# Kernel optimization log

Measured on AMD Instinct MI355X. Metric: run time of the kernel, lower is better.

The kernel has to match this reference:

```python
import jax, jax.numpy as jnp
import numpy as np

D = 256      # embedding_dim
DI = 512     # inner dim = proj_factor * D
H = 4        # num heads
DH = DI // H # head dim
L = 4        # num blocks
K = 4        # causal conv kernel size

def _ln(x, g, b):
    mu = jnp.mean(x, -1, keepdims=True)
    v = jnp.var(x, -1, keepdims=True)
    return (x - mu) * jax.lax.rsqrt(v + 1e-5) * g + b

def _causal_conv(x, w, b):
    # x [B,S,DI], w [K,DI] depthwise causal conv
    S = x.shape[1]
    xp = jnp.pad(x, ((0, 0), (K - 1, 0), (0, 0)))
    out = b
    for j in range(K):
        out = out + xp[:, j:j + S, :] * w[j]
    return out

def _mlstm(q, k, v, ip, fp):
    # parallel stabilized mLSTM. q,k,v [B,S,H,DH]; ip,fp [B,S,H]
    q = q.transpose(0, 2, 1, 3)
    k = k.transpose(0, 2, 1, 3)
    v = v.transpose(0, 2, 1, 3)
    ip = ip.transpose(0, 2, 1)  # [B,H,S]
    fp = fp.transpose(0, 2, 1)
    lf = jax.nn.log_sigmoid(fp)                      # log forget gates
    Fc = jnp.cumsum(lf, axis=-1)
    Fc = jnp.concatenate([jnp.zeros_like(Fc[..., :1]), Fc], axis=-1)  # [B,H,S+1]
    logfg = Fc[..., 1:, None] - Fc[..., None, 1:]    # [B,H,S,S]: sum of log f over (s,t]
    S_len = q.shape[2]
    tri = jnp.tril(jnp.ones((S_len, S_len), dtype=bool))
    logD = jnp.where(tri, logfg + ip[..., None, :], jnp.float32(-1e30))
    m = jnp.max(logD, axis=-1, keepdims=True)        # stabilizer
    Dm = jnp.exp(logD - m)
    qk = jnp.einsum('bhtd,bhsd->bhts', q, k) * (DH ** -0.5)
    C = qk * Dm
    norm = jnp.maximum(jnp.abs(jnp.sum(C, axis=-1, keepdims=True)), jnp.exp(-m))
    h = jnp.einsum('bhts,bhsd->bhtd', C / (norm + 1e-6), v)
    return h.transpose(0, 2, 1, 3)

def _forward(x, time_features, Wp, bp, ln_g, ln_b, Wup, bup, conv_w, conv_b,
             Wq, Wk, Wv, Wif, bif, gn_g, gn_b, skip, Wdown, bdown,
             lnf_g, lnf_b, Wf, bf):
    B, S = x.shape
    xi = jnp.concatenate([x[..., None], time_features], axis=-1)  # [B,S,5]
    h = xi @ Wp + bp                                              # [B,S,D]
    for l in range(L):
        res = h
        hn = _ln(h, ln_g[l], ln_b[l])
        up = hn @ Wup[l] + bup[l]                 # [B,S,2*DI]
        xm, z = up[..., :DI], up[..., DI:]
        xc = jax.nn.silu(_causal_conv(xm, conv_w[l], conv_b[l]))
        q = (xc @ Wq[l]).reshape(B, S, H, DH)
        k = (xc @ Wk[l]).reshape(B, S, H, DH)
        v = (xm @ Wv[l]).reshape(B, S, H, DH)
        gi = jnp.concatenate([q.reshape(B, S, DI), k.reshape(B, S, DI), v.reshape(B, S, DI)], axis=-1)
        gates = gi @ Wif[l] + bif[l]              # [B,S,2H]
        ht = _mlstm(q, k, v, gates[..., :H], gates[..., H:])  # [B,S,H,DH]
        ht = _ln(ht, gn_g[l].reshape(H, DH), gn_b[l].reshape(H, DH)).reshape(B, S, DI)
        ht = ht + skip[l] * xc
        ht = ht * jax.nn.silu(z)
        h = res + ht @ Wdown[l] + bdown[l]
    h = _ln(h, lnf_g, lnf_b)
    return h[:, -1, :] @ Wf + bf                  # [B,1]

def setup_inputs():
    key = jax.random.key(0)
    ks = jax.random.split(key, 16)
    B, S = 8, 1024
    sd = jnp.float32(0.02)
    return {
        'x': jax.random.normal(ks[0], (B, S), jnp.float32),
        'time_features': jax.random.normal(ks[1], (B, S, 4), jnp.float32),
        'Wp': jax.random.normal(ks[2], (5, D)) * sd, 'bp': jnp.zeros((D,)),
        'ln_g': jnp.ones((L, D)), 'ln_b': jnp.zeros((L, D)),
        'Wup': jax.random.normal(ks[3], (L, D, 2 * DI)) * sd, 'bup': jnp.zeros((L, 2 * DI)),
        'conv_w': jax.random.normal(ks[4], (L, K, DI)) * sd, 'conv_b': jnp.zeros((L, DI)),
        'Wq': jax.random.normal(ks[5], (L, DI, DI)) * sd,
        'Wk': jax.random.normal(ks[6], (L, DI, DI)) * sd,
        'Wv': jax.random.normal(ks[7], (L, DI, DI)) * sd,
        'Wif': jax.random.normal(ks[8], (L, 3 * DI, 2 * H)) * sd, 'bif': jnp.zeros((L, 2 * H)),
        'gn_g': jnp.ones((L, DI)), 'gn_b': jnp.zeros((L, DI)),
        'skip': jnp.ones((L, DI)),
        'Wdown': jax.random.normal(ks[9], (L, DI, D)) * sd, 'bdown': jnp.zeros((L, D)),
        'lnf_g': jnp.ones((D,)), 'lnf_b': jnp.zeros((D,)),
        'Wf': jax.random.normal(ks[10], (D, 1)) * sd, 'bf': jnp.zeros((1,)),
    }

def reference(x, time_features, Wp, bp, ln_g, ln_b, Wup, bup, conv_w, conv_b,
              Wq, Wk, Wv, Wif, bif, gn_g, gn_b, skip, Wdown, bdown,
              lnf_g, lnf_b, Wf, bf):
    return _forward(x, time_features, Wp, bp, ln_g, ln_b, Wup, bup, conv_w, conv_b,
                    Wq, Wk, Wv, Wif, bif, gn_g, gn_b, skip, Wdown, bdown,
                    lnf_g, lnf_b, Wf, bf)
```

## Files before the change

### kernel.cpp

```cpp
#include <hip/hip_runtime.h>
#include <hip/hip_bf16.h>
#include <math.h>

#define S 1024
#define NLAYER 4

typedef __bf16 bf16x8 __attribute__((ext_vector_type(8)));
typedef float floatx4 __attribute__((ext_vector_type(4)));

__device__ __forceinline__ float wave_sum(float v) {
  #pragma unroll
  for (int off = 32; off > 0; off >>= 1) v += __shfl_xor(v, off, 64);
  return v;
}

__device__ __forceinline__ void wtrans_body(
    int bid, const float* Wup, const float* Wq, const float* Wk, const float* Wv,
    const float* Wdown, __bf16* WupT, __bf16* WqkT, __bf16* WvT, __bf16* WdownT) {
  __shared__ float T[32][33];
  int layer = bid / 1152, rr = bid % 1152;
  const float* src; __bf16* dst; int K, N, tile;
  if (rr < 256)       { src = Wup   + layer * 262144; dst = WupT  + layer * 262144;          K = 256; N = 1024; tile = rr; }
  else if (rr < 512)  { src = Wq    + layer * 262144; dst = WqkT  + layer * 524288;          K = 512; N = 512;  tile = rr - 256; }
  else if (rr < 768)  { src = Wk    + layer * 262144; dst = WqkT  + layer * 524288 + 262144; K = 512; N = 512;  tile = rr - 512; }
  else if (rr < 1024) { src = Wv    + layer * 262144; dst = WvT   + layer * 262144;          K = 512; N = 512;  tile = rr - 768; }
  else                { src = Wdown + layer * 131072; dst = WdownT + layer * 131072;         K = 512; N = 256;  tile = rr - 1024; }
  int ntn = N >> 5;
  int tk = tile / ntn, tn = tile % ntn;
  int tid = threadIdx.x;
  int r = tid >> 3, c4 = (tid & 7) * 4;
  float4 v = *(const float4*)(src + (size_t)(tk * 32 + r) * N + tn * 32 + c4);
  T[c4 + 0][r] = v.x; T[c4 + 1][r] = v.y; T[c4 + 2][r] = v.z; T[c4 + 3][r] = v.w;
  __syncthreads();
  __bf16 o[4];
  #pragma unroll
  for (int j = 0; j < 4; ++j) o[j] = (__bf16)T[r][c4 + j];
  *(uint2*)(dst + (size_t)(tn * 32 + r) * K + tk * 32 + c4) = *(uint2*)o;
}

__device__ __forceinline__ void wgprep_body(
    int bid, const float* Wq, const float* Wk, const float* Wv,
    const float* Wif, float* wg) {
  int l = bid >> 8;
  int rem = bid & 255;
  int sel = rem >> 7;
  int kg = rem & 127;
  int tid = threadIdx.x;
  int wv = tid >> 6, lane = tid & 63;
  int k = kg * 4 + wv;
  const float* wif = Wif + (size_t)l * 1536 * 8;
  float part[8] = {0, 0, 0, 0, 0, 0, 0, 0};
  if (sel == 0) {
    const float* qr = Wq + (size_t)l * 262144 + (size_t)k * 512;
    const float* kr = Wk + (size_t)l * 262144 + (size_t)k * 512;
    #pragma unroll
    for (int i = 0; i < 8; ++i) {
      int n = lane + i * 64;
      float qv = qr[n], kv = kr[n];
      const float* wq8 = wif + (size_t)n * 8;
      const float* wk8 = wif + (size_t)(512 + n) * 8;
      #pragma unroll
      for (int j = 0; j < 8; ++j) part[j] += qv * wq8[j] + kv * wk8[j];
    }
  } else {
    const float* vr = Wv + (size_t)l * 262144 + (size_t)k * 512;
    #pragma unroll
    for (int i = 0; i < 8; ++i) {
      int n = lane + i * 64;
      float vv = vr[n];
      const float* wv8 = wif + (size_t)(1024 + n) * 8;
      #pragma unroll
      for (int j = 0; j < 8; ++j) part[j] += vv * wv8[j];
    }
  }
  #pragma unroll
  for (int j = 0; j < 8; ++j) part[j] = wave_sum(part[j]);
  if (lane < 8) wg[(size_t)l * 8192 + sel * 4096 + (size_t)k * 8 + lane] = part[lane];
}

__device__ __forceinline__ void embed_body(
    int row, const float* x, const float* tf, const float* Wp, const float* bp,
    const float* g, const float* b, float* h, __bf16* hn) {
  int n = threadIdx.x;
  float xv = x[row];
  const float* t4 = tf + (size_t)row * 4;
  float acc = bp[n] + xv * Wp[n];
  acc += t4[0] * Wp[256 + n];
  acc += t4[1] * Wp[512 + n];
  acc += t4[2] * Wp[768 + n];
  acc += t4[3] * Wp[1024 + n];
  h[(size_t)row * 256 + n] = acc;
  __shared__ float red[4];
  int wid = n >> 6, lane = n & 63;
  float s = wave_sum(acc);
  if (lane == 0) red[wid] = s;
  __syncthreads();
  float mu = (red[0] + red[1] + red[2] + red[3]) * (1.f / 256.f);
  __syncthreads();
  float d = acc - mu;
  float s2 = wave_sum(d * d);
  if (lane == 0) red[wid] = s2;
  __syncthreads();
  float var = (red[0] + red[1] + red[2] + red[3]) * (1.f / 256.f);
  float rs = rsqrtf(var + 1e-5f);
  hn[(size_t)row * 256 + n] = (__bf16)(d * rs * g[n] + b[n]);
}

__global__ __launch_bounds__(256) void prep_kernel(
    const float* __restrict__ x, const float* __restrict__ tf,
    const float* __restrict__ Wp, const float* __restrict__ bp,
    const float* __restrict__ ln_g, const float* __restrict__ ln_b,
    const float* __restrict__ Wup, const float* __restrict__ Wq,
    const float* __restrict__ Wk, const float* __restrict__ Wv,
    const float* __restrict__ Wdown, const float* __restrict__ Wif,
    __bf16* __restrict__ WupT, __bf16* __restrict__ WqkT,
    __bf16* __restrict__ WvT, __bf16* __restrict__ WdownT,
    float* __restrict__ wg, float* __restrict__ h, __bf16* __restrict__ hn) {
  int bid = blockIdx.x;
  if (bid < 4608) {
    wtrans_body(bid, Wup, Wq, Wk, Wv, Wdown, WupT, WqkT, WvT, WdownT);
  } else if (bid < 4608 + 1024) {
    wgprep_body(bid - 4608, Wq, Wk, Wv, Wif, wg);
  } else {
    embed_body(bid - 5632, x, tf, Wp, bp, ln_g, ln_b, h, hn);
  }
}

template <int TM, int MODE, int ACC>
__device__ __forceinline__ void hgemm_body(
    char* smem_raw,
    const __bf16* __restrict__ A, int lda,
    const __bf16* __restrict__ BT, int Kdim,
    const float* __restrict__ bias,
    void* __restrict__ Cout, int ldc, int bxi, int byi) {
  auto As = (__bf16(*)[40])smem_raw;
  auto Bs = (__bf16(*)[40])(smem_raw + (size_t)TM * 80);
  int tid = threadIdx.x;
  int bm = bxi * TM, bn = byi * 128;
  int wid = tid >> 6, lane = tid & 63;
  int wr = wid >> 1, wc = wid & 1;
  int lg = lane >> 4, li = lane & 15;
  constexpr int MI = TM / 32;
  constexpr int WROW = TM / 2;
  floatx4 acc[MI][4];
  #pragma unroll
  for (int i = 0; i < MI; ++i)
    #pragma unroll
    for (int j = 0; j < 4; ++j) acc[i][j] = (floatx4)(0.f);

  int arow = tid >> 2, aseg = tid & 3;
  bf16x8 pa0, pa1, pb0, pb1;
  auto pre = [&](int k0) {
    pa0 = *(const bf16x8*)(A + (size_t)(bm + arow) * lda + k0 + aseg * 8);
    if constexpr (TM == 128)
      pa1 = *(const bf16x8*)(A + (size_t)(bm + arow + 64) * lda + k0 + aseg * 8);
    pb0 = *(const bf16x8*)(BT + (size_t)(bn + arow) * Kdim + k0 + aseg * 8);
    pb1 = *(const bf16x8*)(BT + (size_t)(bn + arow + 64) * Kdim + k0 + aseg * 8);
  };
  pre(0);
  for (int k0 = 0; k0 < Kdim; k0 += 32) {
    __syncthreads();
    *(bf16x8*)&As[arow][aseg * 8] = pa0;
    if constexpr (TM == 128) *(bf16x8*)&As[arow + 64][aseg * 8] = pa1;
    *(bf16x8*)&Bs[arow][aseg * 8] = pb0;
    *(bf16x8*)&Bs[arow + 64][aseg * 8] = pb1;
    __syncthreads();
    if (k0 + 32 < Kdim) pre(k0 + 32);
    bf16x8 af[MI], bfr[4];
    #pragma unroll
    for (int mi = 0; mi < MI; ++mi)
      af[mi] = *(const bf16x8*)&As[wr * WROW + mi * 16 + li][lg * 8];
    #pragma unroll
    for (int ni = 0; ni < 4; ++ni)
      bfr[ni] = *(const bf16x8*)&Bs[wc * 64 + ni * 16 + li][lg * 8];
    #pragma unroll
    for (int mi = 0; mi < MI; ++mi)
      #pragma unroll
      for (int ni = 0; ni < 4; ++ni)
        acc[mi][ni] = __builtin_amdgcn_mfma_f32_16x16x32_bf16(af[mi], bfr[ni], acc[mi][ni], 0, 0, 0);
  }
  if constexpr (MODE == 1) {
    __bf16* eb = (__bf16*)smem_raw;
    const int PITCH = 136;
    __bf16* C = (__bf16*)Cout;
    #pragma unroll
    for (int mi = 0; mi < MI; ++mi) {
      __syncthreads();
      #pragma unroll
      for (int ni = 0; ni < 4; ++ni) {
        int col = wc * 64 + ni * 16 + li;
        float bz = bias ? bias[bn + col] : 0.f;
        #pragma unroll
        for (int r = 0; r < 4; ++r) {
          int lr = wr * 16 + lg * 4 + r;
          eb[lr * PITCH + col] = (__bf16)(acc[mi][ni][r] + bz);
        }
      }
      __syncthreads();
      #pragma unroll
      for (int i = 0; i < 2; ++i) {
        int lr = (tid >> 4) + i * 16;
        int c8 = (tid & 15) * 8;
        bf16x8 v = *(const bf16x8*)&eb[lr * PITCH + c8];
        int row_g = bm + (lr >> 4) * 64 + mi * 16 + (lr & 15);
        *(bf16x8*)(C + (size_t)row_g * ldc + bn + c8) = v;
      }
    }
  } else {
    #pragma unroll
    for (int mi = 0; mi < MI; ++mi) {
      int row = bm + wr * WROW + mi * 16 + lg * 4;
      #pragma unroll
      for (int ni = 0; ni < 4; ++ni) {
        int col = bn + wc * 64 + ni * 16 + li;
        if constexpr (MODE == 2) {
          __bf16 o4[4];
          #pragma unroll
          for (int r = 0; r < 4; ++r) o4[r] = (__bf16)acc[mi][ni][r];
          __bf16* vt = (__bf16*)Cout;
          size_t off = ((size_t)((row >> 10) * 4 + (col >> 7)) * 128 + (col & 127)) * 1024 + (row & 1023);
          *(uint2*)(vt + off) = *(uint2*)o4;
        } else {
          float bz = bias ? bias[col] : 0.f;
          float* C = (float*)Cout;
          #pragma unroll
          for (int r = 0; r < 4; ++r) {
            float v = acc[mi][ni][r] + bz;
            if (ACC) v += C[(size_t)(row + r) * ldc + col];
            C[(size_t)(row + r) * ldc + col] = v;
          }
        }
      }
    }
  }
}

template <int TM, int MODE, int ACC>
__global__ __launch_bounds__(256) void hgemm(
    const __bf16* __restrict__ A, int lda,
    const __bf16* __restrict__ BT, int Kdim,
    const float* __restrict__ bias,
    void* __restrict__ Cout, int ldc) {
  extern __shared__ char smem[];
  hgemm_body<TM, MODE, ACC>(smem, A, lda, BT, Kdim, bias, Cout, ldc,
                            blockIdx.x, blockIdx.y);
}

__device__ __forceinline__ void scan_body(
    int bh, int lane, const float* __restrict__ gates, float* __restrict__ gout,
    float* __restrict__ Mout, float* __restrict__ NFout) {
  int bb = bh >> 2, hh = bh & 3;
  float ip[16], pf[16];
  #pragma unroll
  for (int i = 0; i < 16; ++i) {
    int t = lane * 16 + i;
    const float* grow = gates + ((size_t)(bb * S + t)) * 8;
    ip[i] = grow[hh];
    float fp = grow[4 + hh];
    float lf = fminf(fp, 0.f) - log1pf(__expf(-fabsf(fp)));
    pf[i] = (i == 0) ? lf : pf[i - 1] + lf;
  }
  float T = pf[15];
  float inc = T;
  #pragma unroll
  for (int off = 1; off < 64; off <<= 1) {
    float v = __shfl_up(inc, off, 64);
    if (lane >= off) inc += v;
  }
  float excl = inc - T;
  float F[16], g[16], pm[16];
  #pragma unroll
  for (int i = 0; i < 16; ++i) {
    F[i] = excl + pf[i];
    g[i] = ip[i] - F[i];
    pm[i] = (i == 0) ? g[0] : fmaxf(pm[i - 1], g[i]);
  }
  float Mx = pm[15];
  float incm = Mx;
  #pragma unroll
  for (int off = 1; off < 64; off <<= 1) {
    float v = __shfl_up(incm, off, 64);
    if (lane >= off) incm = fmaxf(incm, v);
  }
  float em = __shfl_up(incm, 1, 64);
  if (lane == 0) em = -3.4e38f;
  #pragma unroll
  for (int i = 0; i < 16; ++i) {
    int t = lane * 16 + i;
    size_t o = (size_t)bh * S + t;
    float M = fmaxf(em, pm[i]);
    gout[o] = g[i];
    Mout[o] = M;
    NFout[o] = __expf(-F[i] - M);
  }
}

__global__ __launch_bounds__(256) void qkv_kernel(
    const __bf16* __restrict__ xc, const __bf16* __restrict__ WqkT,
    __bf16* __restrict__ qk, const __bf16* __restrict__ up,
    const __bf16* __restrict__ WvT, __bf16* __restrict__ vT,
    const float* __restrict__ gates, float* __restrict__ gbuf,
    float* __restrict__ Mbuf, float* __restrict__ NFbuf) {
  extern __shared__ char smem[];
  if (blockIdx.y < 8) {
    hgemm_body<128, 1, 0>(smem, xc, 512, WqkT, 512, nullptr, qk, 1024,
                          blockIdx.x, blockIdx.y);
  } else if (blockIdx.y < 16) {
    int j = blockIdx.y - 8;
    hgemm_body<64, 2, 0>(smem, up, 1024, WvT, 512, nullptr, vT, 0,
                         blockIdx.x * 2 + (j & 1), j >> 1);
  } else {
    if (blockIdx.x < 32 && threadIdx.x < 64)
      scan_body(blockIdx.x, threadIdx.x, gates, gbuf, Mbuf, NFbuf);
  }
}

__global__ __launch_bounds__(256) void dgemm_ln_kernel(
    const __bf16* __restrict__ A, const __bf16* __restrict__ BT,
    const float* __restrict__ bias, float* __restrict__ h,
    const float* __restrict__ lng, const float* __restrict__ lnb,
    __bf16* __restrict__ hn) {
  __shared__ __bf16 As[32][40];
  __shared__ __bf16 Bs[256][40];
  __shared__ float redS[2][32], redQ[2][32];
  int tid = threadIdx.x;
  int bm = blockIdx.x * 32;
  int wid = tid >> 6, lane = tid & 63;
  int wr = wid >> 1, wc = wid & 1;
  int lg = lane >> 4, li = lane & 15;
  floatx4 acc[8];
  #pragma unroll
  for (int j = 0; j < 8; ++j) acc[j] = (floatx4)(0.f);

  int arow = tid >> 2, aseg = tid & 3;
  bf16x8 pa, pb[4];
  auto pre = [&](int k0) {
    if (tid < 128)
      pa = *(const bf16x8*)(A + (size_t)(bm + arow) * 512 + k0 + aseg * 8);
    #pragma unroll
    for (int i = 0; i < 4; ++i)
      pb[i] = *(const bf16x8*)(BT + (size_t)(arow + i * 64) * 512 + k0 + aseg * 8);
  };
  pre(0);
  for (int k0 = 0; k0 < 512; k0 += 32) {
    __syncthreads();
    if (tid < 128) *(bf16x8*)&As[arow][aseg * 8] = pa;
    #pragma unroll
    for (int i = 0; i < 4; ++i) *(bf16x8*)&Bs[arow + i * 64][aseg * 8] = pb[i];
    __syncthreads();
    if (k0 + 32 < 512) pre(k0 + 32);
    bf16x8 af = *(const bf16x8*)&As[wr * 16 + li][lg * 8];
    #pragma unroll
    for (int ni = 0; ni < 8; ++ni) {
      bf16x8 bfr = *(const bf16x8*)&Bs[wc * 128 + ni * 16 + li][lg * 8];
      acc[ni] = __builtin_amdgcn_mfma_f32_16x16x32_bf16(af, bfr, acc[ni], 0, 0, 0);
    }
  }
  #pragma unroll
  for (int r = 0; r < 4; ++r) {
    int lr = wr * 16 + lg * 4 + r;
    int row = bm + lr;
    float s1 = 0.f, s2 = 0.f;
    #pragma unroll
    for (int ni = 0; ni < 8; ++ni) {
      int col = wc * 128 + ni * 16 + li;
      float v = acc[ni][r] + bias[col] + h[(size_t)row * 256 + col];
      acc[ni][r] = v;
      h[(size_t)row * 256 + col] = v;
      s1 += v;
      s2 += v * v;
    }
    s1 += __shfl_xor(s1, 1, 64); s1 += __shfl_xor(s1, 2, 64);
    s1 += __shfl_xor(s1, 4, 64); s1 += __shfl_xor(s1, 8, 64);
    s2 += __shfl_xor(s2, 1, 64); s2 += __shfl_xor(s2, 2, 64);
    s2 += __shfl_xor(s2, 4, 64); s2 += __shfl_xor(s2, 8, 64);
    if (li == 0) { redS[wc][lr] = s1; redQ[wc][lr] = s2; }
  }
  if (!lng) return;
  __syncthreads();
  #pragma unroll
  for (int r = 0; r < 4; ++r) {
    int lr = wr * 16 + lg * 4 + r;
    int row = bm + lr;
    float s1 = redS[0][lr] + redS[1][lr];
    float s2 = redQ[0][lr] + redQ[1][lr];
    float mu = s1 * (1.f / 256.f);
    float var = s2 * (1.f / 256.f) - mu * mu;
    float rs = rsqrtf(var + 1e-5f);
    #pragma unroll
    for (int ni = 0; ni < 8; ++ni) {
      int col = wc * 128 + ni * 16 + li;
      hn[(size_t)row * 256 + col] = (__bf16)((acc[ni][r] - mu) * rs * lng[col] + lnb[col]);
    }
  }
}

__global__ __launch_bounds__(256) void conv_silu_kernel(
    const __bf16* __restrict__ up, const float* __restrict__ cw,
    const float* __restrict__ cb, const float* __restrict__ wg,
    const float* __restrict__ bif, __bf16* __restrict__ xc,
    float* __restrict__ gates) {
  int tid = threadIdx.x;
  int wv = tid >> 6, lane = tid & 63;
  int row = blockIdx.x * 4 + wv;
  int c8 = lane * 8;
  int t = row & (S - 1);
  float acc[8];
  *(float4*)&acc[0] = *(const float4*)(cb + c8);
  *(float4*)&acc[4] = *(const float4*)(cb + c8 + 4);
  float xm[8];
  #pragma unroll
  for (int j = 0; j < 4; ++j) {
    int tt = t - 3 + j;
    if (tt >= 0) {
      bf16x8 xv = *(const bf16x8*)(up + (size_t)(row - 3 + j) * 1024 + c8);
      float4 w0 = *(const float4*)(cw + j * 512 + c8);
      float4 w1 = *(const float4*)(cw + j * 512 + c8 + 4);
      acc[0] += w0.x * (float)xv[0]; acc[1] += w0.y * (float)xv[1];
      acc[2] += w0.z * (float)xv[2]; acc[3] += w0.w * (float)xv[3];
      acc[4] += w1.x * (float)xv[4]; acc[5] += w1.y * (float)xv[5];
      acc[6] += w1.z * (float)xv[6]; acc[7] += w1.w * (float)xv[7];
      if (j == 3) {
        #pragma unroll
        for (int m = 0; m < 8; ++m) xm[m] = (float)xv[m];
      }
    }
  }
  bf16x8 o;
  float xcs[8];
  #pragma unroll
  for (int m = 0; m < 8; ++m) {
    float sg = 1.f / (1.f + __expf(-acc[m]));
    xcs[m] = acc[m] * sg;
    o[m] = (__bf16)xcs[m];
  }
  *(bf16x8*)(xc + (size_t)row * 512 + c8) = o;
  const float* w1 = wg + (size_t)c8 * 8;
  const float* w2 = wg + 4096 + (size_t)c8 * 8;
  float part[8] = {0, 0, 0, 0, 0, 0, 0, 0};
  #pragma unroll
  for (int m = 0; m < 8; ++m) {
    const float* a = w1 + m * 8;
    const float* b = w2 + m * 8;
    #pragma unroll
    for (int j = 0; j < 8; ++j) part[j] += xcs[m] * a[j] + xm[m] * b[j];
  }
  #pragma unroll
  for (int j = 0; j < 8; ++j) part[j] = wave_sum(part[j]);
  if (lane < 8) gates[(size_t)row * 8 + lane] = part[lane] + bif[lane];
}

__global__ __launch_bounds__(512, 1) void attn_kernel(
    const __bf16* __restrict__ qk, const __bf16* __restrict__ vT,
    const float* __restrict__ gbuf, const float* __restrict__ Mbuf,
    const float* __restrict__ NFbuf,
    const float* __restrict__ gn_g, const float* __restrict__ gn_b,
    const float* __restrict__ skip,
    const __bf16* __restrict__ xc, const __bf16* __restrict__ up,
    __bf16* __restrict__ hd) {
  __shared__ __bf16 Ks[64][136];
  __shared__ __bf16 Vs[128][72];
  __shared__ __bf16 plds[8][16][72];
  __shared__ float gls[64];
  __shared__ float glds[128], blds[128], slds[128];
  int px = blockIdx.y, bh = blockIdx.x;
  int tqA = px, tqB = 15 - px;
  int bb = bh >> 2, hh = bh & 3;
  int tid = threadIdx.x;
  int wv = tid >> 6, lane = tid & 63;
  int sel = wv >> 2, wl = wv & 3;
  int lg = lane >> 4, li = lane & 15;
  int tq = (sel == 0) ? tqA : tqB;
  int tb = tq * 64 + wl * 16;
  const float scale = 0.08838834764831845f;

  if (tid < 128) {
    glds[tid] = gn_g[hh * 128 + tid];
    blds[tid] = gn_b[hh * 128 + tid];
    slds[tid] = skip[hh * 128 + tid];
  }

  bf16x8 aq[4];
  {
    const __bf16* qp = qk + ((size_t)(bb * S + tb + li)) * 1024 + hh * 128 + lg * 8;
    #pragma unroll
    for (int cd = 0; cd < 4; ++cd) aq[cd] = *(const bf16x8*)(qp + cd * 32);
  }
  float ml[4], nf[4];
  #pragma unroll
  for (int r = 0; r < 4; ++r) {
    ml[r] = Mbuf[(size_t)bh * S + tb + lg * 4 + r];
    nf[r] = NFbuf[(size_t)bh * S + tb + lg * 4 + r];
  }

  floatx4 oacc[8];
  #pragma unroll
  for (int df = 0; df < 8; ++df) oacc[df] = (floatx4)(0.f);
  float rs[4] = {0, 0, 0, 0};

  int krow = tid >> 3, kcol = tid & 7;
  bf16x8 kreg0, kreg1, vreg0, vreg1;
  float greg = 0.f;
  auto preload = [&](int st) {
    int s0 = st * 64;
    const __bf16* kp = qk + ((size_t)(bb * S + s0 + krow)) * 1024 + 512 + hh * 128;
    kreg0 = *(const bf16x8*)(kp + kcol * 8);
    kreg1 = *(const bf16x8*)(kp + 64 + kcol * 8);
    vreg0 = *(const bf16x8*)(vT + ((size_t)(bh * 128 + krow)) * 1024 + s0 + kcol * 8);
    vreg1 = *(const bf16x8*)(vT + ((size_t)(bh * 128 + 64 + krow)) * 1024 + s0 + kcol * 8);
    if (tid < 64) greg = gbuf[(size_t)bh * S + s0 + tid];
  };
  preload(0);

  for (int st = 0; st <= tqB; ++st) {
    __syncthreads();
    *(bf16x8*)&Ks[krow][kcol * 8] = kreg0;
    *(bf16x8*)&Ks[krow][64 + kcol * 8] = kreg1;
    *(bf16x8*)&Vs[krow][kcol * 8] = vreg0;
    *(bf16x8*)&Vs[64 + krow][kcol * 8] = vreg1;
    if (tid < 64) gls[tid] = greg;
    __syncthreads();
    if (st < tqB) preload(st + 1);

    if (st <= tq) {
      int s0 = st * 64;
      #pragma unroll
      for (int ns = 0; ns < 4; ++ns) {
        bf16x8 bk0 = *(const bf16x8*)&Ks[ns * 16 + li][lg * 8];
        bf16x8 bk1 = *(const bf16x8*)&Ks[ns * 16 + li][32 + lg * 8];
        bf16x8 bk2 = *(const bf16x8*)&Ks[ns * 16 + li][64 + lg * 8];
        bf16x8 bk3 = *(const bf16x8*)&Ks[ns * 16 + li][96 + lg * 8];
        int s = s0 + ns * 16 + li;
        float gv = gls[ns * 16 + li];
        floatx4 pa = (floatx4)(0.f);
        pa = __builtin_amdgcn_mfma_f32_16x16x32_bf16(aq[0], bk0, pa, 0, 0, 0);
        pa = __builtin_amdgcn_mfma_f32_16x16x32_bf16(aq[1], bk1, pa, 0, 0, 0);
        pa = __builtin_amdgcn_mfma_f32_16x16x32_bf16(aq[2], bk2, pa, 0, 0, 0);
        pa = __builtin_amdgcn_mfma_f32_16x16x32_bf16(aq[3], bk3, pa, 0, 0, 0);
        #pragma unroll
        for (int r = 0; r < 4; ++r) {
          int t = tb + lg * 4 + r;
          float val = pa[r] * scale * __expf(gv - ml[r]);
          float w = (s <= t) ? val : 0.f;
          rs[r] += w;
          plds[wv][lg * 4 + r][ns * 16 + li] = (__bf16)w;
        }
      }
      bf16x8 ap0 = *(const bf16x8*)&plds[wv][li][lg * 8];
      bf16x8 ap1 = *(const bf16x8*)&plds[wv][li][32 + lg * 8];
      #pragma unroll
      for (int df = 0; df < 8; ++df) {
        bf16x8 bv0 = *(const bf16x8*)&Vs[df * 16 + li][lg * 8];
        bf16x8 bv1 = *(const bf16x8*)&Vs[df * 16 + li][32 + lg * 8];
        oacc[df] = __builtin_amdgcn_mfma_f32_16x16x32_bf16(ap0, bv0, oacc[df], 0, 0, 0);
        oacc[df] = __builtin_amdgcn_mfma_f32_16x16x32_bf16(ap1, bv1, oacc[df], 0, 0, 0);
      }
    }
  }
  #pragma unroll
  for (int r = 0; r < 4; ++r) {
    float a = rs[r];
    a += __shfl_xor(a, 1, 64); a += __shfl_xor(a, 2, 64);
    a += __shfl_xor(a, 4, 64); a += __shfl_xor(a, 8, 64);
    rs[r] = a;
  }
  #pragma unroll
  for (int r = 0; r < 4; ++r) {
    float inv = 1.f / (fmaxf(fabsf(rs[r]), nf[r]) + 1e-6f);
    float v8[8], s1 = 0.f, s2 = 0.f;
    #pragma unroll
    for (int df = 0; df < 8; ++df) {
      float v = oacc[df][r] * inv;
      v8[df] = v;
      s1 += v;
      s2 += v * v;
    }
    s1 += __shfl_xor(s1, 1, 64); s1 += __shfl_xor(s1, 2, 64);
    s1 += __shfl_xor(s1, 4, 64); s1 += __shfl_xor(s1, 8, 64);
    s2 += __shfl_xor(s2, 1, 64); s2 += __shfl_xor(s2, 2, 64);
    s2 += __shfl_xor(s2, 4, 64); s2 += __shfl_xor(s2, 8, 64);
    float mu = s1 * (1.f / 128.f);
    float var = s2 * (1.f / 128.f) - mu * mu;
    float rq = rsqrtf(var + 1e-5f);
    int t = tb + lg * 4 + r;
    const __bf16* xr = xc + ((size_t)(bb * S + t)) * 512 + hh * 128 + li;
    const __bf16* zr = up + ((size_t)(bb * S + t)) * 1024 + 512 + hh * 128 + li;
    __bf16* od = hd + ((size_t)(bb * S + t)) * 512 + hh * 128 + li;
    #pragma unroll
    for (int df = 0; df < 8; ++df) {
      int c = df * 16 + li;
      float ln = (v8[df] - mu) * rq * glds[c] + blds[c];
      float val = ln + slds[c] * (float)xr[df * 16];
      float z = (float)zr[df * 16];
      float sg = 1.f / (1.f + __expf(-z));
      od[df * 16] = (__bf16)(val * (z * sg));
    }
  }
}

__global__ __launch_bounds__(256) void final_kernel(
    const float* __restrict__ h, const float* __restrict__ g,
    const float* __restrict__ b, const float* __restrict__ Wf,
    const float* __restrict__ bf, float* __restrict__ out) {
  int bb = blockIdx.x, tid = threadIdx.x;
  size_t row = (size_t)(bb * S + S - 1) * 256;
  __shared__ float red[4];
  float v = h[row + tid];
  float s = wave_sum(v);
  int wid = tid >> 6, lane = tid & 63;
  if (lane == 0) red[wid] = s;
  __syncthreads();
  float mu = (red[0] + red[1] + red[2] + red[3]) * (1.f / 256.f);
  __syncthreads();
  float d = v - mu;
  float s2 = wave_sum(d * d);
  if (lane == 0) red[wid] = s2;
  __syncthreads();
  float var = (red[0] + red[1] + red[2] + red[3]) * (1.f / 256.f);
  float rs = rsqrtf(var + 1e-5f);
  float ln = d * rs * g[tid] + b[tid];
  float p = ln * Wf[tid];
  float psum = wave_sum(p);
  __syncthreads();
  if (lane == 0) red[wid] = psum;
  __syncthreads();
  if (tid == 0) out[bb] = red[0] + red[1] + red[2] + red[3] + bf[0];
}

extern "C" void kernel_launch(void* const* d_in, const int* in_sizes, int n_in,
                              void* d_out, int out_size, void* d_ws, size_t ws_size,
                              hipStream_t stream) {
  const float* x      = (const float*)d_in[0];
  const float* tf     = (const float*)d_in[1];
  const float* Wp     = (const float*)d_in[2];
  const float* bp     = (const float*)d_in[3];
  const float* ln_g   = (const float*)d_in[4];
  const float* ln_b   = (const float*)d_in[5];
  const float* Wup    = (const float*)d_in[6];
  const float* bup    = (const float*)d_in[7];
  const float* conv_w = (const float*)d_in[8];
  const float* conv_b = (const float*)d_in[9];
  const float* Wq     = (const float*)d_in[10];
  const float* Wk     = (const float*)d_in[11];
  const float* Wv     = (const float*)d_in[12];
  const float* Wif    = (const float*)d_in[13];
  const float* bif    = (const float*)d_in[14];
  const float* gn_g   = (const float*)d_in[15];
  const float* gn_b   = (const float*)d_in[16];
  const float* skip   = (const float*)d_in[17];
  const float* Wdown  = (const float*)d_in[18];
  const float* bdown  = (const float*)d_in[19];
  const float* lnf_g  = (const float*)d_in[20];
  const float* lnf_b  = (const float*)d_in[21];
  const float* Wf     = (const float*)d_in[22];
  const float* bf     = (const float*)d_in[23];
  float* out = (float*)d_out;

  float* h     = (float*)d_ws;
  float* gates = h + 2097152;
  float* gbuf  = gates + 65536;
  float* Mbuf  = gbuf + 32768;
  float* NFbuf = Mbuf + 32768;
  float* wgbuf = NFbuf + 32768;
  __bf16* hn   = (__bf16*)(wgbuf + 32768);
  __bf16* up   = hn + 2097152;
  __bf16* xc   = up + 8388608;
  __bf16* qk   = xc + 4194304;
  __bf16* vT   = qk + 8388608;
  __bf16* hd   = vT + 4194304;
  __bf16* WupT   = hd + 4194304;
  __bf16* WqkT   = WupT + 1048576;
  __bf16* WvT    = WqkT + 2097152;
  __bf16* WdownT = WvT + 1048576;

  prep_kernel<<<13824, 256, 0, stream>>>(
      x, tf, Wp, bp, ln_g, ln_b, Wup, Wq, Wk, Wv, Wdown, Wif,
      WupT, WqkT, WvT, WdownT, wgbuf, h, hn);
  for (int l = 0; l < NLAYER; ++l) {
    hgemm<128, 1, 0><<<dim3(64, 8), 256, 20480, stream>>>(
        hn, 256, WupT + (size_t)l * 262144, 256, bup + l * 1024, up, 1024);
    conv_silu_kernel<<<2048, 256, 0, stream>>>(up, conv_w + l * 2048, conv_b + l * 512,
                                               wgbuf + l * 8192, bif + l * 8, xc, gates);
    qkv_kernel<<<dim3(64, 17), 256, 20480, stream>>>(
        xc, WqkT + (size_t)l * 524288, qk, up, WvT + (size_t)l * 262144, vT,
        gates, gbuf, Mbuf, NFbuf);
    attn_kernel<<<dim3(32, 8), 512, 0, stream>>>(
        qk, vT, gbuf, Mbuf, NFbuf, gn_g + l * 512, gn_b + l * 512, skip + l * 512,
        xc, up, hd);
    const float* lng = (l + 1 < NLAYER) ? (ln_g + (l + 1) * 256) : nullptr;
    const float* lnb = (l + 1 < NLAYER) ? (ln_b + (l + 1) * 256) : nullptr;
    dgemm_ln_kernel<<<256, 256, 0, stream>>>(
        hd, WdownT + (size_t)l * 131072, bdown + l * 256, h, lng, lnb, hn);
  }
  final_kernel<<<8, 256, 0, stream>>>(h, lnf_g, lnf_b, Wf, bf, out);
}
```

Baseline: 619.4 us.

## Double-buffer LDS in GEMM mainloops and fuse final head into last dgemm

The hgemm and dgemm_ln mainloops switch to double-buffered shared memory, so the next K-tile is written into the alternate buffer after the MFMAs and each iteration needs one barrier instead of two. Dynamic shared memory for hgemm doubles to 40 KB, which may lower occupancy. The final LayerNorm and projection for the last token of each sequence now run in the epilogue of the last-layer dgemm_ln, and the separate final_kernel launch is removed.

```diff
diff --git a/kernel.cpp b/kernel.cpp
--- a/kernel.cpp
+++ b/kernel.cpp
@@ -134,7 +134,7 @@
     const float* __restrict__ bias,
     void* __restrict__ Cout, int ldc, int bxi, int byi) {
   auto As = (__bf16(*)[40])smem_raw;
-  auto Bs = (__bf16(*)[40])(smem_raw + (size_t)TM * 80);
+  auto Bs = (__bf16(*)[40])(smem_raw + (size_t)TM * 160);
   int tid = threadIdx.x;
   int bm = bxi * TM, bn = byi * 128;
   int wid = tid >> 6, lane = tid & 63;
@@ -157,27 +157,35 @@
     pb0 = *(const bf16x8*)(BT + (size_t)(bn + arow) * Kdim + k0 + aseg * 8);
     pb1 = *(const bf16x8*)(BT + (size_t)(bn + arow + 64) * Kdim + k0 + aseg * 8);
   };
+  auto stor = [&](int buf) {
+    *(bf16x8*)&As[buf * TM + arow][aseg * 8] = pa0;
+    if constexpr (TM == 128) *(bf16x8*)&As[buf * TM + arow + 64][aseg * 8] = pa1;
+    *(bf16x8*)&Bs[buf * 128 + arow][aseg * 8] = pb0;
+    *(bf16x8*)&Bs[buf * 128 + arow + 64][aseg * 8] = pb1;
+  };
   pre(0);
+  stor(0);
+  if (32 < Kdim) pre(32);
+  int cur = 0;
   for (int k0 = 0; k0 < Kdim; k0 += 32) {
     __syncthreads();
-    *(bf16x8*)&As[arow][aseg * 8] = pa0;
-    if constexpr (TM == 128) *(bf16x8*)&As[arow + 64][aseg * 8] = pa1;
-    *(bf16x8*)&Bs[arow][aseg * 8] = pb0;
-    *(bf16x8*)&Bs[arow + 64][aseg * 8] = pb1;
-    __syncthreads();
-    if (k0 + 32 < Kdim) pre(k0 + 32);
     bf16x8 af[MI], bfr[4];
     #pragma unroll
     for (int mi = 0; mi < MI; ++mi)
-      af[mi] = *(const bf16x8*)&As[wr * WROW + mi * 16 + li][lg * 8];
+      af[mi] = *(const bf16x8*)&As[cur * TM + wr * WROW + mi * 16 + li][lg * 8];
     #pragma unroll
     for (int ni = 0; ni < 4; ++ni)
-      bfr[ni] = *(const bf16x8*)&Bs[wc * 64 + ni * 16 + li][lg * 8];
+      bfr[ni] = *(const bf16x8*)&Bs[cur * 128 + wc * 64 + ni * 16 + li][lg * 8];
     #pragma unroll
     for (int mi = 0; mi < MI; ++mi)
       #pragma unroll
       for (int ni = 0; ni < 4; ++ni)
         acc[mi][ni] = __builtin_amdgcn_mfma_f32_16x16x32_bf16(af[mi], bfr[ni], acc[mi][ni], 0, 0, 0);
+    if (k0 + 32 < Kdim) {
+      stor(cur ^ 1);
+      if (k0 + 64 < Kdim) pre(k0 + 64);
+    }
+    cur ^= 1;
   }
   if constexpr (MODE == 1) {
     __bf16* eb = (__bf16*)smem_raw;
@@ -319,9 +327,12 @@
     const __bf16* __restrict__ A, const __bf16* __restrict__ BT,
     const float* __restrict__ bias, float* __restrict__ h,
     const float* __restrict__ lng, const float* __restrict__ lnb,
-    __bf16* __restrict__ hn) {
-  __shared__ __bf16 As[32][40];
-  __shared__ __bf16 Bs[256][40];
+    __bf16* __restrict__ hn,
+    const float* __restrict__ lnfg, const float* __restrict__ lnfb,
+    const float* __restrict__ Wf, const float* __restrict__ bf,
+    float* __restrict__ out) {
+  __shared__ __bf16 As[2 * 32][40];
+  __shared__ __bf16 Bs[2 * 256][40];
   __shared__ float redS[2][32], redQ[2][32];
   int tid = threadIdx.x;
   int bm = blockIdx.x * 32;
@@ -341,20 +352,29 @@
     for (int i = 0; i < 4; ++i)
       pb[i] = *(const bf16x8*)(BT + (size_t)(arow + i * 64) * 512 + k0 + aseg * 8);
   };
+  auto stor = [&](int buf) {
+    if (tid < 128) *(bf16x8*)&As[buf * 32 + arow][aseg * 8] = pa;
+    #pragma unroll
+    for (int i = 0; i < 4; ++i)
+      *(bf16x8*)&Bs[buf * 256 + arow + i * 64][aseg * 8] = pb[i];
+  };
   pre(0);
+  stor(0);
+  pre(32);
+  int cur = 0;
   for (int k0 = 0; k0 < 512; k0 += 32) {
     __syncthreads();
-    if (tid < 128) *(bf16x8*)&As[arow][aseg * 8] = pa;
-    #pragma unroll
-    for (int i = 0; i < 4; ++i) *(bf16x8*)&Bs[arow + i * 64][aseg * 8] = pb[i];
-    __syncthreads();
-    if (k0 + 32 < 512) pre(k0 + 32);
-    bf16x8 af = *(const bf16x8*)&As[wr * 16 + li][lg * 8];
+    bf16x8 af = *(const bf16x8*)&As[cur * 32 + wr * 16 + li][lg * 8];
     #pragma unroll
     for (int ni = 0; ni < 8; ++ni) {
-      bf16x8 bfr = *(const bf16x8*)&Bs[wc * 128 + ni * 16 + li][lg * 8];
+      bf16x8 bfr = *(const bf16x8*)&Bs[cur * 256 + wc * 128 + ni * 16 + li][lg * 8];
       acc[ni] = __builtin_amdgcn_mfma_f32_16x16x32_bf16(af, bfr, acc[ni], 0, 0, 0);
     }
+    if (k0 + 32 < 512) {
+      stor(cur ^ 1);
+      if (k0 + 64 < 512) pre(k0 + 64);
+    }
+    cur ^= 1;
   }
   #pragma unroll
   for (int r = 0; r < 4; ++r) {
@@ -376,22 +396,43 @@
     s2 += __shfl_xor(s2, 4, 64); s2 += __shfl_xor(s2, 8, 64);
     if (li == 0) { redS[wc][lr] = s1; redQ[wc][lr] = s2; }
   }
-  if (!lng) return;
   __syncthreads();
-  #pragma unroll
-  for (int r = 0; r < 4; ++r) {
-    int lr = wr * 16 + lg * 4 + r;
-    int row = bm + lr;
-    float s1 = redS[0][lr] + redS[1][lr];
-    float s2 = redQ[0][lr] + redQ[1][lr];
-    float mu = s1 * (1.f / 256.f);
-    float var = s2 * (1.f / 256.f) - mu * mu;
-    float rs = rsqrtf(var + 1e-5f);
-    #pragma unroll
-    for (int ni = 0; ni < 8; ++ni) {
-      int col = wc * 128 + ni * 16 + li;
-      hn[(size_t)row * 256 + col] = (__bf16)((acc[ni][r] - mu) * rs * lng[col] + lnb[col]);
-    }
+  if (lng) {
+    #pragma unroll
+    for (int r = 0; r < 4; ++r) {
+      int lr = wr * 16 + lg * 4 + r;
+      int row = bm + lr;
+      float s1 = redS[0][lr] + redS[1][lr];
+      float s2 = redQ[0][lr] + redQ[1][lr];
+      float mu = s1 * (1.f / 256.f);
+      float var = s2 * (1.f / 256.f) - mu * mu;
+      float rs = rsqrtf(var + 1e-5f);
+      #pragma unroll
+      for (int ni = 0; ni < 8; ++ni) {
+        int col = wc * 128 + ni * 16 + li;
+        hn[(size_t)row * 256 + col] = (__bf16)((acc[ni][r] - mu) * rs * lng[col] + lnb[col]);
+      }
+    }
+  } else if ((bm & 1023) == 992) {
+    if (wr == 1 && lg == 3) {
+      float s1 = redS[0][31] + redS[1][31];
+      float s2 = redQ[0][31] + redQ[1][31];
+      float mu = s1 * (1.f / 256.f);
+      float var = s2 * (1.f / 256.f) - mu * mu;
+      float rs = rsqrtf(var + 1e-5f);
+      float p = 0.f;
+      #pragma unroll
+      for (int ni = 0; ni < 8; ++ni) {
+        int col = wc * 128 + ni * 16 + li;
+        float ln = (acc[ni][3] - mu) * rs * lnfg[col] + lnfb[col];
+        p += ln * Wf[col];
+      }
+      p += __shfl_xor(p, 1, 64); p += __shfl_xor(p, 2, 64);
+      p += __shfl_xor(p, 4, 64); p += __shfl_xor(p, 8, 64);
+      if (li == 0) redS[wc][0] = p;
+    }
+    __syncthreads();
+    if (tid == 0) out[bm >> 10] = redS[0][0] + redS[1][0] + bf[0];
   }
 }
 
@@ -596,35 +637,6 @@
       od[df * 16] = (__bf16)(val * (z * sg));
     }
   }
-}
-
-__global__ __launch_bounds__(256) void final_kernel(
-    const float* __restrict__ h, const float* __restrict__ g,
-    const float* __restrict__ b, const float* __restrict__ Wf,
-    const float* __restrict__ bf, float* __restrict__ out) {
-  int bb = blockIdx.x, tid = threadIdx.x;
-  size_t row = (size_t)(bb * S + S - 1) * 256;
-  __shared__ float red[4];
-  float v = h[row + tid];
-  float s = wave_sum(v);
-  int wid = tid >> 6, lane = tid & 63;
-  if (lane == 0) red[wid] = s;
-  __syncthreads();
-  float mu = (red[0] + red[1] + red[2] + red[3]) * (1.f / 256.f);
-  __syncthreads();
-  float d = v - mu;
-  float s2 = wave_sum(d * d);
-  if (lane == 0) red[wid] = s2;
-  __syncthreads();
-  float var = (red[0] + red[1] + red[2] + red[3]) * (1.f / 256.f);
-  float rs = rsqrtf(var + 1e-5f);
-  float ln = d * rs * g[tid] + b[tid];
-  float p = ln * Wf[tid];
-  float psum = wave_sum(p);
-  __syncthreads();
-  if (lane == 0) red[wid] = psum;
-  __syncthreads();
-  if (tid == 0) out[bb] = red[0] + red[1] + red[2] + red[3] + bf[0];
 }
 
 extern "C" void kernel_launch(void* const* d_in, const int* in_sizes, int n_in,
@@ -677,11 +689,11 @@
       x, tf, Wp, bp, ln_g, ln_b, Wup, Wq, Wk, Wv, Wdown, Wif,
       WupT, WqkT, WvT, WdownT, wgbuf, h, hn);
   for (int l = 0; l < NLAYER; ++l) {
-    hgemm<128, 1, 0><<<dim3(64, 8), 256, 20480, stream>>>(
+    hgemm<128, 1, 0><<<dim3(64, 8), 256, 40960, stream>>>(
         hn, 256, WupT + (size_t)l * 262144, 256, bup + l * 1024, up, 1024);
     conv_silu_kernel<<<2048, 256, 0, stream>>>(up, conv_w + l * 2048, conv_b + l * 512,
                                                wgbuf + l * 8192, bif + l * 8, xc, gates);
-    qkv_kernel<<<dim3(64, 17), 256, 20480, stream>>>(
+    qkv_kernel<<<dim3(64, 17), 256, 40960, stream>>>(
         xc, WqkT + (size_t)l * 524288, qk, up, WvT + (size_t)l * 262144, vT,
         gates, gbuf, Mbuf, NFbuf);
     attn_kernel<<<dim3(32, 8), 512, 0, stream>>>(
@@ -690,7 +702,7 @@
     const float* lng = (l + 1 < NLAYER) ? (ln_g + (l + 1) * 256) : nullptr;
     const float* lnb = (l + 1 < NLAYER) ? (ln_b + (l + 1) * 256) : nullptr;
     dgemm_ln_kernel<<<256, 256, 0, stream>>>(
-        hd, WdownT + (size_t)l * 131072, bdown + l * 256, h, lng, lnb, hn);
-  }
-  final_kernel<<<8, 256, 0, stream>>>(h, lnf_g, lnf_b, Wf, bf, out);
-}
+        hd, WdownT + (size_t)l * 131072, bdown + l * 256, h, lng, lnb, hn,
+        lnf_g, lnf_b, Wf, bf, out);
+  }
+}
```

Result: faster. 593.9 us (-4.1%).
